# Optimization experiments

Measured on AMD Instinct MI355X. Metric: run time of the kernel, lower is better.

The kernel has to match this reference:

```python
import jax, jax.numpy as jnp
import numpy as np

N_NODES = 50000
N_EDGES = 800000
IN_DIM = 256
HID = 32
HEADS = 8
OUT_DIM = 16
NEG_SLOPE = 0.2


def setup_inputs() -> dict:
    key = jax.random.key(0)
    ks = jax.random.split(key, 12)
    s = 0.05
    return {
        "emb": jax.random.normal(ks[0], (N_NODES, IN_DIM), jnp.float32),
        "src": jax.random.randint(ks[1], (N_EDGES,), 0, N_NODES),
        "dst": jax.random.randint(ks[2], (N_EDGES,), 0, N_NODES),
        "W1": jax.random.normal(ks[3], (IN_DIM, HEADS * HID), jnp.float32) * s,
        "attn_l1": jax.random.normal(ks[4], (HEADS, HID), jnp.float32) * s,
        "attn_r1": jax.random.normal(ks[5], (HEADS, HID), jnp.float32) * s,
        "bias1": jax.random.normal(ks[6], (HEADS * HID,), jnp.float32) * s,
        "W2": jax.random.normal(ks[7], (HEADS * HID, OUT_DIM), jnp.float32) * s,
        "attn_l2": jax.random.normal(ks[8], (1, OUT_DIM), jnp.float32) * s,
        "attn_r2": jax.random.normal(ks[9], (1, OUT_DIM), jnp.float32) * s,
        "bias2": jax.random.normal(ks[10], (OUT_DIM,), jnp.float32) * s,
    }


def gat_conv(x, src, dst, W, attn_l, attn_r, bias, n_heads, d_out):
    # x: [N, F_in] -> per-head projection h: [N, H, D]
    n = x.shape[0]
    h = (x @ W).reshape(n, n_heads, d_out)
    el = jnp.sum(h * attn_l, axis=-1)  # [N, H]
    er = jnp.sum(h * attn_r, axis=-1)  # [N, H]
    # edge scores with LeakyReLU (DGL negative_slope=0.2)
    e = jax.nn.leaky_relu(el[src] + er[dst], NEG_SLOPE)  # [E, H]
    # edge softmax over incoming edges of each destination node
    m = jax.ops.segment_max(e, dst, num_segments=n)  # [N, H]
    ee = jnp.exp(e - m[dst])
    denom = jax.ops.segment_sum(ee, dst, num_segments=n)  # [N, H]
    alpha = ee / denom[dst]  # [E, H]
    # weighted scatter-sum aggregation
    out = jax.ops.segment_sum(h[src] * alpha[:, :, None], dst, num_segments=n)  # [N, H, D]
    return out + bias.reshape(1, n_heads, d_out)


def reference(emb, src, dst, W1, attn_l1, attn_r1, bias1, W2, attn_l2, attn_r2, bias2):
    h = gat_conv(emb, src, dst, W1, attn_l1, attn_r1, bias1, HEADS, HID)  # [N, 8, 32]
    h = jax.nn.elu(h.reshape(N_NODES, HEADS * HID))  # [N, 256]
    out = gat_conv(h, src, dst, W2, attn_l2, attn_r2, bias2, 1, OUT_DIM)  # [N, 1, 16]
    return jnp.squeeze(out, axis=1)  # [N, 16]
```

## Files before the change

### kernel.cpp

```cpp
#include <hip/hip_runtime.h>
#include <math.h>

#define N_NODES 50000
#define N_EDGES 800000
#define NEG_SLOPE 0.2f

typedef __attribute__((ext_vector_type(8))) short bf16x8;
typedef __attribute__((ext_vector_type(4))) float f32x4;
typedef __attribute__((ext_vector_type(4))) _Float16 half4;

__device__ inline unsigned short f32_to_bf16_rn(float x) {
    unsigned u = __builtin_bit_cast(unsigned, x);
    unsigned r = u + 0x7fffu + ((u >> 16) & 1u);
    return (unsigned short)(r >> 16);
}
__device__ inline float bf16_bits_to_f32(unsigned short h) {
    unsigned u = ((unsigned)h) << 16;
    return __builtin_bit_cast(float, u);
}


__global__ void count_deg(const int* __restrict__ dst, int* __restrict__ deg) {
    int i = blockIdx.x * 256 + threadIdx.x;
    if (i < N_EDGES) atomicAdd(&deg[dst[i]], 1);
}

__global__ void scan_block(const int* __restrict__ deg, int* __restrict__ tmp,
                           int* __restrict__ bsum) {
    __shared__ int buf[256];
    int tid = threadIdx.x;
    int i = blockIdx.x * 256 + tid;
    int v = (i < N_NODES) ? deg[i] : 0;
    buf[tid] = v;
    __syncthreads();
    for (int off = 1; off < 256; off <<= 1) {
        int x = (tid >= off) ? buf[tid - off] : 0;
        __syncthreads();
        buf[tid] += x;
        __syncthreads();
    }
    if (i < N_NODES) tmp[i] = buf[tid];
    if (tid == 255) bsum[blockIdx.x] = buf[255];
}

__global__ void scan_bsum(int* __restrict__ bsum, int nb) {
    __shared__ int buf[256];
    int tid = threadIdx.x;
    int v = (tid < nb) ? bsum[tid] : 0;
    buf[tid] = v;
    __syncthreads();
    for (int off = 1; off < 256; off <<= 1) {
        int x = (tid >= off) ? buf[tid - off] : 0;
        __syncthreads();
        buf[tid] += x;
        __syncthreads();
    }
    if (tid < nb) bsum[tid] = buf[tid] - v;
}

__global__ void finalize_offs(const int* __restrict__ tmp, const int* __restrict__ deg,
                              const int* __restrict__ bsum, int* __restrict__ offs,
                              int* __restrict__ cursor) {
    int i = blockIdx.x * 256 + threadIdx.x;
    if (i < N_NODES) {
        int incl = tmp[i] + bsum[i >> 8];
        offs[i + 1] = incl;
        cursor[i] = incl - deg[i];
        if (i == 0) offs[0] = 0;
    }
}

__global__ void scatter_edges(const int* __restrict__ src, const int* __restrict__ dst,
                              int* __restrict__ cursor, int* __restrict__ src_csr) {
    int i = blockIdx.x * 256 + threadIdx.x;
    if (i < N_EDGES) {
        int p = atomicAdd(&cursor[dst[i]], 1);
        src_csr[p] = src[i];
    }
}


__global__ void convert_W1T(const float* __restrict__ W,
                            unsigned short* __restrict__ Th,
                            unsigned short* __restrict__ Tl) {
    int n = blockIdx.x;
    int k = threadIdx.x;
    float x = W[k * 256 + n];
    unsigned short h = f32_to_bf16_rn(x);
    float lo = x - bf16_bits_to_f32(h);
    size_t idx = ((size_t)(k >> 3) * 256 + n) * 8 + (k & 7);
    Th[idx] = h;
    Tl[idx] = f32_to_bf16_rn(lo);
}


__global__ __launch_bounds__(256) void gemm1_fused(const float* __restrict__ A,
                                                   const unsigned short* __restrict__ BTh,
                                                   const unsigned short* __restrict__ BTl,
                                                   const float* __restrict__ al,
                                                   const float* __restrict__ ar,
                                                   _Float16* __restrict__ C,
                                                   float* __restrict__ el,
                                                   float* __restrict__ er, int M) {
    __shared__ unsigned short Ah[4][64][8], Al[4][64][8];
    __shared__ unsigned short Bh[4][256][8], Bl[4][256][8];
    int tid = threadIdx.x;
    int lane = tid & 63, wave = tid >> 6;
    int kgl = lane >> 4, rl = lane & 15;
    int row0 = blockIdx.x * 64;

    f32x4 acc[4][4];
#pragma unroll
    for (int i = 0; i < 4; i++)
#pragma unroll
        for (int j = 0; j < 4; j++) acc[i][j] = (f32x4){0.f, 0.f, 0.f, 0.f};

    for (int k0 = 0; k0 < 256; k0 += 32) {
        {
            int row = tid >> 2, kg = tid & 3;
            int gr = row0 + row;
            float4 x0 = make_float4(0.f, 0.f, 0.f, 0.f);
            float4 x1 = make_float4(0.f, 0.f, 0.f, 0.f);
            if (gr < M) {
                const float* p = &A[(size_t)gr * 256 + k0 + kg * 8];
                x0 = *reinterpret_cast<const float4*>(p);
                x1 = *reinterpret_cast<const float4*>(p + 4);
            }
            float xs[8] = {x0.x, x0.y, x0.z, x0.w, x1.x, x1.y, x1.z, x1.w};
            unsigned short hs[8], ls[8];
#pragma unroll
            for (int j = 0; j < 8; j++) {
                hs[j] = f32_to_bf16_rn(xs[j]);
                ls[j] = f32_to_bf16_rn(xs[j] - bf16_bits_to_f32(hs[j]));
            }
            *reinterpret_cast<bf16x8*>(&Ah[kg][row][0]) = *reinterpret_cast<bf16x8*>(hs);
            *reinterpret_cast<bf16x8*>(&Al[kg][row][0]) = *reinterpret_cast<bf16x8*>(ls);
        }
        int s0 = k0 >> 3;
#pragma unroll
        for (int i = 0; i < 4; i++) {
            const unsigned short* ph = &BTh[((size_t)(s0 + i) * 256 + tid) * 8];
            const unsigned short* pl = &BTl[((size_t)(s0 + i) * 256 + tid) * 8];
            *reinterpret_cast<bf16x8*>(&Bh[i][tid][0]) = *reinterpret_cast<const bf16x8*>(ph);
            *reinterpret_cast<bf16x8*>(&Bl[i][tid][0]) = *reinterpret_cast<const bf16x8*>(pl);
        }
        __syncthreads();
        bf16x8 a_h[4], a_l[4];
#pragma unroll
        for (int mf = 0; mf < 4; mf++) {
            int row = mf * 16 + rl;
            a_h[mf] = *reinterpret_cast<bf16x8*>(&Ah[kgl][row][0]);
            a_l[mf] = *reinterpret_cast<bf16x8*>(&Al[kgl][row][0]);
        }
#pragma unroll
        for (int nf = 0; nf < 4; nf++) {
            int col = wave * 64 + nf * 16 + rl;
            bf16x8 bh = *reinterpret_cast<bf16x8*>(&Bh[kgl][col][0]);
            bf16x8 bl = *reinterpret_cast<bf16x8*>(&Bl[kgl][col][0]);
#pragma unroll
            for (int mf = 0; mf < 4; mf++) {
                acc[mf][nf] = __builtin_amdgcn_mfma_f32_16x16x32_bf16(a_h[mf], bh, acc[mf][nf], 0, 0, 0);
                acc[mf][nf] = __builtin_amdgcn_mfma_f32_16x16x32_bf16(a_h[mf], bl, acc[mf][nf], 0, 0, 0);
                acc[mf][nf] = __builtin_amdgcn_mfma_f32_16x16x32_bf16(a_l[mf], bh, acc[mf][nf], 0, 0, 0);
            }
        }
        __syncthreads();
    }
    float alv[4], arv[4];
#pragma unroll
    for (int nf = 0; nf < 4; nf++) {
        int c = wave * 64 + nf * 16 + rl;
        alv[nf] = al[c];
        arv[nf] = ar[c];
    }
#pragma unroll
    for (int mf = 0; mf < 4; mf++) {
#pragma unroll
        for (int rr = 0; rr < 4; rr++) {
            int grow = row0 + mf * 16 + (lane >> 4) * 4 + rr;
            bool ok = grow < M;
            if (ok) {
#pragma unroll
                for (int nf = 0; nf < 4; nf++) {
                    int gcol = wave * 64 + nf * 16 + rl;
                    C[(size_t)grow * 256 + gcol] = (_Float16)acc[mf][nf][rr];
                }
            }
            float e0 = acc[mf][0][rr] * alv[0] + acc[mf][1][rr] * alv[1];
            float e1 = acc[mf][2][rr] * alv[2] + acc[mf][3][rr] * alv[3];
            float f0 = acc[mf][0][rr] * arv[0] + acc[mf][1][rr] * arv[1];
            float f1 = acc[mf][2][rr] * arv[2] + acc[mf][3][rr] * arv[3];
#pragma unroll
            for (int off = 8; off >= 1; off >>= 1) {
                e0 += __shfl_down(e0, off, 16);
                e1 += __shfl_down(e1, off, 16);
                f0 += __shfl_down(f0, off, 16);
                f1 += __shfl_down(f1, off, 16);
            }
            if (rl == 0 && ok) {
                int h0 = wave * 2;
                el[grow * 8 + h0] = e0;
                el[grow * 8 + h0 + 1] = e1;
                er[grow * 8 + h0] = f0;
                er[grow * 8 + h0 + 1] = f1;
            }
        }
    }
}


__global__ __launch_bounds__(64) void agg1_fused(const int* __restrict__ offs,
                                                 const int* __restrict__ src_csr,
                                                 const float* __restrict__ el,
                                                 const float* __restrict__ er,
                                                 const _Float16* __restrict__ h1h,
                                                 const float* __restrict__ bias1,
                                                 _Float16* __restrict__ x2) {
    __shared__ float sc[64][8];
    int v = blockIdx.x;
    int t = threadIdx.x;
    int head = t >> 3, slot = t & 7;
    int start = offs[v], end = offs[v + 1];
    int deg = end - start;
    int ncache = (deg < 64) ? deg : 64;
    float erv = er[v * 8 + head];
    float s = 0.f;
    for (int base = 0; base < ncache; base += 8) {
        int e = base + slot;
        if (e < ncache) {
            int u = src_csr[start + e];
            float x = el[u * 8 + head] + erv;
            x = (x >= 0.f) ? x : NEG_SLOPE * x;
            float ex = expf(x);
            sc[e][head] = ex;
            s += ex;
        }
    }
    for (int base = 64; base < deg; base += 8) {
        int e = base + slot;
        if (e < deg) {
            int u = src_csr[start + e];
            float x = el[u * 8 + head] + erv;
            x = (x >= 0.f) ? x : NEG_SLOPE * x;
            s += expf(x);
        }
    }
    s += __shfl_xor(s, 1);
    s += __shfl_xor(s, 2);
    s += __shfl_xor(s, 4);
    float invs = (s > 0.f) ? 1.f / s : 0.f;
    __syncthreads();
    float4 acc = make_float4(0.f, 0.f, 0.f, 0.f);
    int i = start;
    for (; i + 3 < end && (i - start) + 3 < 64; i += 4) {
        int e = i - start;
        int u0 = src_csr[i];
        int u1 = src_csr[i + 1];
        int u2 = src_csr[i + 2];
        int u3 = src_csr[i + 3];
        float a0 = sc[e][head] * invs;
        float a1 = sc[e + 1][head] * invs;
        float a2 = sc[e + 2][head] * invs;
        float a3 = sc[e + 3][head] * invs;
        half4 p0 = *reinterpret_cast<const half4*>(&h1h[(size_t)u0 * 256 + 4 * t]);
        half4 p1 = *reinterpret_cast<const half4*>(&h1h[(size_t)u1 * 256 + 4 * t]);
        half4 p2 = *reinterpret_cast<const half4*>(&h1h[(size_t)u2 * 256 + 4 * t]);
        half4 p3 = *reinterpret_cast<const half4*>(&h1h[(size_t)u3 * 256 + 4 * t]);
        acc.x += a0 * (float)p0[0] + a1 * (float)p1[0] + a2 * (float)p2[0] + a3 * (float)p3[0];
        acc.y += a0 * (float)p0[1] + a1 * (float)p1[1] + a2 * (float)p2[1] + a3 * (float)p3[1];
        acc.z += a0 * (float)p0[2] + a1 * (float)p1[2] + a2 * (float)p2[2] + a3 * (float)p3[2];
        acc.w += a0 * (float)p0[3] + a1 * (float)p1[3] + a2 * (float)p2[3] + a3 * (float)p3[3];
    }
    for (; i < end; i++) {
        int e = i - start;
        int u0 = src_csr[i];
        float a0;
        if (e < 64) {
            a0 = sc[e][head] * invs;
        } else {
            float x = el[u0 * 8 + head] + erv;
            x = (x >= 0.f) ? x : NEG_SLOPE * x;
            a0 = expf(x) * invs;
        }
        half4 p0 = *reinterpret_cast<const half4*>(&h1h[(size_t)u0 * 256 + 4 * t]);
        acc.x += a0 * (float)p0[0];
        acc.y += a0 * (float)p0[1];
        acc.z += a0 * (float)p0[2];
        acc.w += a0 * (float)p0[3];
    }
    float4 b = *reinterpret_cast<const float4*>(&bias1[4 * t]);
    float ox = acc.x + b.x, oy = acc.y + b.y, oz = acc.z + b.z, ow = acc.w + b.w;
    ox = (ox > 0.f) ? ox : (expf(ox) - 1.f);
    oy = (oy > 0.f) ? oy : (expf(oy) - 1.f);
    oz = (oz > 0.f) ? oz : (expf(oz) - 1.f);
    ow = (ow > 0.f) ? ow : (expf(ow) - 1.f);
    half4 o = {(_Float16)ox, (_Float16)oy, (_Float16)oz, (_Float16)ow};
    *reinterpret_cast<half4*>(&x2[(size_t)v * 256 + 4 * t]) = o;
}


__global__ __launch_bounds__(256) void gemm2_elr(const _Float16* __restrict__ X,
                                                 const float* __restrict__ W,
                                                 const float* __restrict__ al,
                                                 const float* __restrict__ ar,
                                                 float* __restrict__ h2,
                                                 float* __restrict__ el2,
                                                 float* __restrict__ er2) {
    __shared__ float Ws[16 * 260];
    __shared__ float Xs[16][260];
    int tid = threadIdx.x;
    for (int i = tid; i < 256 * 16; i += 256) {
        int k = i >> 4, c = i & 15;
        Ws[c * 260 + k] = W[i];
    }
    int row0 = blockIdx.x * 16;
#pragma unroll
    for (int i = 0; i < 4; i++) {
        int idx = tid + 256 * i;
        int r = idx >> 6, c4 = idx & 63;
        half4 xv = *reinterpret_cast<const half4*>(&X[(size_t)(row0 + r) * 256 + c4 * 4]);
        Xs[r][c4 * 4 + 0] = (float)xv[0];
        Xs[r][c4 * 4 + 1] = (float)xv[1];
        Xs[r][c4 * 4 + 2] = (float)xv[2];
        Xs[r][c4 * 4 + 3] = (float)xv[3];
    }
    __syncthreads();
    int r = tid >> 4, c = tid & 15;
    float acc = 0.f;
#pragma unroll
    for (int k = 0; k < 256; k += 4) {
        float4 xv = *reinterpret_cast<const float4*>(&Xs[r][k]);
        float4 wv = *reinterpret_cast<const float4*>(&Ws[c * 260 + k]);
        acc += xv.x * wv.x + xv.y * wv.y + xv.z * wv.z + xv.w * wv.w;
    }
    h2[(size_t)(row0 + r) * 16 + c] = acc;
    float pl = acc * al[c], pr = acc * ar[c];
    for (int off = 8; off >= 1; off >>= 1) {
        pl += __shfl_down(pl, off, 16);
        pr += __shfl_down(pr, off, 16);
    }
    if (c == 0) {
        el2[row0 + r] = pl;
        er2[row0 + r] = pr;
    }
}


__global__ __launch_bounds__(64) void agg2_fused(const int* __restrict__ offs,
                                                 const int* __restrict__ src_csr,
                                                 const float* __restrict__ el2,
                                                 const float* __restrict__ er2,
                                                 const float* __restrict__ h2,
                                                 const float* __restrict__ bias2,
                                                 float* __restrict__ out) {
    int v = blockIdx.x;
    int t = threadIdx.x;
    int start = offs[v], end = offs[v + 1];
    float erv = er2[v];
    float s = 0.f;
    for (int i = start + t; i < end; i += 64) {
        int u = src_csr[i];
        float x = el2[u] + erv;
        x = (x >= 0.f) ? x : NEG_SLOPE * x;
        s += expf(x);
    }
#pragma unroll
    for (int off = 32; off >= 1; off >>= 1) s += __shfl_xor(s, off);
    float invs = (s > 0.f) ? 1.f / s : 0.f;
    int eg = t >> 4, d = t & 15;
    float acc = 0.f;
    for (int i = start + eg; i < end; i += 4) {
        int u = src_csr[i];
        float x = el2[u] + erv;
        x = (x >= 0.f) ? x : NEG_SLOPE * x;
        acc += expf(x) * invs * h2[(size_t)u * 16 + d];
    }
    acc += __shfl_xor(acc, 32);
    acc += __shfl_xor(acc, 16);
    if (t < 16) out[(size_t)v * 16 + t] = acc + bias2[t];
}


extern "C" void kernel_launch(void* const* d_in, const int* in_sizes, int n_in,
                              void* d_out, int out_size, void* d_ws, size_t ws_size,
                              hipStream_t stream) {
    const float* emb   = (const float*)d_in[0];
    const int*   src   = (const int*)d_in[1];
    const int*   dst   = (const int*)d_in[2];
    const float* W1    = (const float*)d_in[3];
    const float* al1   = (const float*)d_in[4];
    const float* ar1   = (const float*)d_in[5];
    const float* bias1 = (const float*)d_in[6];
    const float* W2    = (const float*)d_in[7];
    const float* al2   = (const float*)d_in[8];
    const float* ar2   = (const float*)d_in[9];
    const float* bias2 = (const float*)d_in[10];
    float* out = (float*)d_out;

    char* ws = (char*)d_ws;
    auto alloc = [&](size_t bytes) -> void* {
        void* p = ws;
        ws += (bytes + 255) & ~(size_t)255;
        return p;
    };
    int* deg     = (int*)alloc(N_NODES * 4);
    int* cursor  = (int*)alloc(N_NODES * 4);
    int* offs    = (int*)alloc((N_NODES + 1) * 4);
    int* tmp     = (int*)alloc(N_NODES * 4);
    int* bsum    = (int*)alloc(256 * 4);
    int* src_csr = (int*)alloc(N_EDGES * 4);
    unsigned short* W1Th = (unsigned short*)alloc(256 * 256 * 2);
    unsigned short* W1Tl = (unsigned short*)alloc(256 * 256 * 2);
    _Float16* h1h = (_Float16*)alloc((size_t)N_NODES * 256 * 2);
    float* el1   = (float*)alloc(N_NODES * 8 * 4);
    float* er1   = (float*)alloc(N_NODES * 8 * 4);
    _Float16* x2h = (_Float16*)alloc((size_t)N_NODES * 256 * 2);
    float* h2    = (float*)alloc((size_t)N_NODES * 16 * 4);
    float* el2   = (float*)alloc(N_NODES * 4);
    float* er2   = (float*)alloc(N_NODES * 4);

    int nb = (N_NODES + 255) / 256;

    hipMemsetAsync(deg, 0, N_NODES * 4, stream);
    count_deg<<<(N_EDGES + 255) / 256, 256, 0, stream>>>(dst, deg);
    scan_block<<<nb, 256, 0, stream>>>(deg, tmp, bsum);
    scan_bsum<<<1, 256, 0, stream>>>(bsum, nb);
    finalize_offs<<<nb, 256, 0, stream>>>(tmp, deg, bsum, offs, cursor);
    scatter_edges<<<(N_EDGES + 255) / 256, 256, 0, stream>>>(src, dst, cursor, src_csr);

    convert_W1T<<<256, 256, 0, stream>>>(W1, W1Th, W1Tl);
    gemm1_fused<<<(N_NODES + 63) / 64, 256, 0, stream>>>(emb, W1Th, W1Tl, al1, ar1,
                                                         h1h, el1, er1, N_NODES);
    agg1_fused<<<N_NODES, 64, 0, stream>>>(offs, src_csr, el1, er1, h1h, bias1, x2h);
    gemm2_elr<<<N_NODES / 16, 256, 0, stream>>>(x2h, W2, al2, ar2, h2, el2, er2);
    agg2_fused<<<N_NODES, 64, 0, stream>>>(offs, src_csr, el2, er2, h2, bias2, out);
}
```

Baseline: 259.6 us.

## Use MFMA split-bf16 for second GEMM and direct-to-LDS B loads in first

Replaces the scalar FP32 LDS dot-product gemm2 with an MFMA kernel. It splits both operands into hi/lo bf16 halves and accumulates three MFMA products to keep near-FP32 accuracy. Each block now handles 64 rows instead of 16, and the el/er reductions are done through lane shuffles on the MFMA output layout. Separately, gemm1 now moves its W1 tile loads straight into LDS with global_load_lds, issued before the A conversion, to skip the register round trip and overlap with the A work. The cost is extra conversion arithmetic in gemm2 and reliance on correct waitcnt handling before the barrier for the async LDS loads.

```diff
diff --git a/kernel.cpp b/kernel.cpp
--- a/kernel.cpp
+++ b/kernel.cpp
@@ -17,6 +17,11 @@
 __device__ inline float bf16_bits_to_f32(unsigned short h) {
     unsigned u = ((unsigned)h) << 16;
     return __builtin_bit_cast(float, u);
+}
+__device__ inline void load_lds16(const void* g, void* l) {
+    __builtin_amdgcn_global_load_lds(
+        (const __attribute__((address_space(1))) void*)g,
+        (__attribute__((address_space(3))) void*)l, 16, 0, 0);
 }
 
 
@@ -116,6 +121,12 @@
         for (int j = 0; j < 4; j++) acc[i][j] = (f32x4){0.f, 0.f, 0.f, 0.f};
 
     for (int k0 = 0; k0 < 256; k0 += 32) {
+        int s0 = k0 >> 3;
+#pragma unroll
+        for (int i = 0; i < 4; i++) {
+            load_lds16(&BTh[((size_t)(s0 + i) * 256 + tid) * 8], &Bh[i][wave << 6][0]);
+            load_lds16(&BTl[((size_t)(s0 + i) * 256 + tid) * 8], &Bl[i][wave << 6][0]);
+        }
         {
             int row = tid >> 2, kg = tid & 3;
             int gr = row0 + row;
@@ -135,14 +146,6 @@
             }
             *reinterpret_cast<bf16x8*>(&Ah[kg][row][0]) = *reinterpret_cast<bf16x8*>(hs);
             *reinterpret_cast<bf16x8*>(&Al[kg][row][0]) = *reinterpret_cast<bf16x8*>(ls);
-        }
-        int s0 = k0 >> 3;
-#pragma unroll
-        for (int i = 0; i < 4; i++) {
-            const unsigned short* ph = &BTh[((size_t)(s0 + i) * 256 + tid) * 8];
-            const unsigned short* pl = &BTl[((size_t)(s0 + i) * 256 + tid) * 8];
-            *reinterpret_cast<bf16x8*>(&Bh[i][tid][0]) = *reinterpret_cast<const bf16x8*>(ph);
-            *reinterpret_cast<bf16x8*>(&Bl[i][tid][0]) = *reinterpret_cast<const bf16x8*>(pl);
         }
         __syncthreads();
         bf16x8 a_h[4], a_l[4];
@@ -299,49 +302,83 @@
 }
 
 
-__global__ __launch_bounds__(256) void gemm2_elr(const _Float16* __restrict__ X,
-                                                 const float* __restrict__ W,
-                                                 const float* __restrict__ al,
-                                                 const float* __restrict__ ar,
-                                                 float* __restrict__ h2,
-                                                 float* __restrict__ el2,
-                                                 float* __restrict__ er2) {
-    __shared__ float Ws[16 * 260];
-    __shared__ float Xs[16][260];
+__global__ __launch_bounds__(256) void gemm2_mfma(const _Float16* __restrict__ X,
+                                                  const float* __restrict__ W2,
+                                                  const float* __restrict__ al,
+                                                  const float* __restrict__ ar,
+                                                  float* __restrict__ h2,
+                                                  float* __restrict__ el2,
+                                                  float* __restrict__ er2, int M) {
+    __shared__ unsigned short Xh[4][64][8], Xl[4][64][8];
+    __shared__ unsigned short Wh[32][16][8], Wl[32][16][8];
     int tid = threadIdx.x;
-    for (int i = tid; i < 256 * 16; i += 256) {
-        int k = i >> 4, c = i & 15;
-        Ws[c * 260 + k] = W[i];
-    }
-    int row0 = blockIdx.x * 16;
-#pragma unroll
-    for (int i = 0; i < 4; i++) {
-        int idx = tid + 256 * i;
-        int r = idx >> 6, c4 = idx & 63;
-        half4 xv = *reinterpret_cast<const half4*>(&X[(size_t)(row0 + r) * 256 + c4 * 4]);
-        Xs[r][c4 * 4 + 0] = (float)xv[0];
-        Xs[r][c4 * 4 + 1] = (float)xv[1];
-        Xs[r][c4 * 4 + 2] = (float)xv[2];
-        Xs[r][c4 * 4 + 3] = (float)xv[3];
+    int lane = tid & 63, wave = tid >> 6;
+    int kgl = lane >> 4, rl = lane & 15;
+    int row0 = blockIdx.x * 64;
+
+#pragma unroll
+    for (int j = 0; j < 16; j++) {
+        int e = tid * 16 + j;
+        float x = W2[e];
+        unsigned short h = f32_to_bf16_rn(x);
+        unsigned short l = f32_to_bf16_rn(x - bf16_bits_to_f32(h));
+        int k = e >> 4, c = e & 15;
+        Wh[k >> 3][c][k & 7] = h;
+        Wl[k >> 3][c][k & 7] = l;
     }
     __syncthreads();
-    int r = tid >> 4, c = tid & 15;
-    float acc = 0.f;
-#pragma unroll
-    for (int k = 0; k < 256; k += 4) {
-        float4 xv = *reinterpret_cast<const float4*>(&Xs[r][k]);
-        float4 wv = *reinterpret_cast<const float4*>(&Ws[c * 260 + k]);
-        acc += xv.x * wv.x + xv.y * wv.y + xv.z * wv.z + xv.w * wv.w;
-    }
-    h2[(size_t)(row0 + r) * 16 + c] = acc;
-    float pl = acc * al[c], pr = acc * ar[c];
-    for (int off = 8; off >= 1; off >>= 1) {
-        pl += __shfl_down(pl, off, 16);
-        pr += __shfl_down(pr, off, 16);
-    }
-    if (c == 0) {
-        el2[row0 + r] = pl;
-        er2[row0 + r] = pr;
+
+    f32x4 acc = (f32x4){0.f, 0.f, 0.f, 0.f};
+    for (int k0 = 0; k0 < 256; k0 += 32) {
+        {
+            int row = tid >> 2, kg = tid & 3;
+            int gr = row0 + row;
+            unsigned short hs[8], ls[8];
+            if (gr < M) {
+                half4 x0 = *reinterpret_cast<const half4*>(&X[(size_t)gr * 256 + k0 + kg * 8]);
+                half4 x1 = *reinterpret_cast<const half4*>(&X[(size_t)gr * 256 + k0 + kg * 8 + 4]);
+                float xs[8] = {(float)x0[0], (float)x0[1], (float)x0[2], (float)x0[3],
+                               (float)x1[0], (float)x1[1], (float)x1[2], (float)x1[3]};
+#pragma unroll
+                for (int j = 0; j < 8; j++) {
+                    hs[j] = f32_to_bf16_rn(xs[j]);
+                    ls[j] = f32_to_bf16_rn(xs[j] - bf16_bits_to_f32(hs[j]));
+                }
+            } else {
+#pragma unroll
+                for (int j = 0; j < 8; j++) { hs[j] = 0; ls[j] = 0; }
+            }
+            *reinterpret_cast<bf16x8*>(&Xh[kg][row][0]) = *reinterpret_cast<bf16x8*>(hs);
+            *reinterpret_cast<bf16x8*>(&Xl[kg][row][0]) = *reinterpret_cast<bf16x8*>(ls);
+        }
+        __syncthreads();
+        bf16x8 a_h = *reinterpret_cast<bf16x8*>(&Xh[kgl][wave * 16 + rl][0]);
+        bf16x8 a_l = *reinterpret_cast<bf16x8*>(&Xl[kgl][wave * 16 + rl][0]);
+        int kg = (k0 >> 3) + kgl;
+        bf16x8 b_h = *reinterpret_cast<bf16x8*>(&Wh[kg][rl][0]);
+        bf16x8 b_l = *reinterpret_cast<bf16x8*>(&Wl[kg][rl][0]);
+        acc = __builtin_amdgcn_mfma_f32_16x16x32_bf16(a_h, b_h, acc, 0, 0, 0);
+        acc = __builtin_amdgcn_mfma_f32_16x16x32_bf16(a_h, b_l, acc, 0, 0, 0);
+        acc = __builtin_amdgcn_mfma_f32_16x16x32_bf16(a_l, b_h, acc, 0, 0, 0);
+        __syncthreads();
+    }
+    float alv = al[rl], arv = ar[rl];
+#pragma unroll
+    for (int rr = 0; rr < 4; rr++) {
+        int grow = row0 + wave * 16 + (lane >> 4) * 4 + rr;
+        bool ok = grow < M;
+        if (ok) h2[(size_t)grow * 16 + rl] = acc[rr];
+        float pl = acc[rr] * alv;
+        float pr = acc[rr] * arv;
+#pragma unroll
+        for (int off = 8; off >= 1; off >>= 1) {
+            pl += __shfl_down(pl, off, 16);
+            pr += __shfl_down(pr, off, 16);
+        }
+        if (rl == 0 && ok) {
+            el2[grow] = pl;
+            er2[grow] = pr;
+        }
     }
 }
 
@@ -432,6 +469,6 @@
     gemm1_fused<<<(N_NODES + 63) / 64, 256, 0, stream>>>(emb, W1Th, W1Tl, al1, ar1,
                                                          h1h, el1, er1, N_NODES);
     agg1_fused<<<N_NODES, 64, 0, stream>>>(offs, src_csr, el1, er1, h1h, bias1, x2h);
-    gemm2_elr<<<N_NODES / 16, 256, 0, stream>>>(x2h, W2, al2, ar2, h2, el2, er2);
+    gemm2_mfma<<<(N_NODES + 63) / 64, 256, 0, stream>>>(x2h, W2, al2, ar2, h2, el2, er2, N_NODES);
     agg2_fused<<<N_NODES, 64, 0, stream>>>(offs, src_csr, el2, er2, h2, bias2, out);
 }
```

Result: faster. 254.4 us (-2.0%).
